# Kernel tuning notes

Hardware: AMD Instinct MI355X
Metric: run time of the kernel (lower is better)

## Reference

```python
import jax, jax.numpy as jnp
import numpy as np

KH = KW = 3
PAD = 1
SPE = 16  # msfa 4x4

def _unfold(x):
    # torch F.unfold order: feature index = c*(kh*kw) + di*kw + dj
    N, C, H, W = x.shape
    xp = jnp.pad(x, ((0, 0), (0, 0), (PAD, PAD), (PAD, PAD)))
    patches = jnp.stack(
        [xp[:, :, di:di + H, dj:dj + W] for di in range(KH) for dj in range(KW)],
        axis=2,
    )  # [N, C, KH*KW, H, W]
    return patches.reshape(N, C * KH * KW, H * W)

def setup_inputs() -> dict:
    key = jax.random.key(0)
    k1, k2 = jax.random.split(key)
    x = jax.random.normal(k1, (4, 32, 256, 256), dtype=jnp.float32)
    # kaiming_uniform(a=sqrt(5)) on fan_in = in_channels*kh*kw of the (spe,K,outC) tensor;
    # exact init distribution is irrelevant for correctness baseline, use scaled uniform.
    fan_in = 288
    bound = np.sqrt(6.0 / ((1 + 5) * fan_in))
    weight = jax.random.uniform(k2, (SPE, 288, 64), dtype=jnp.float32, minval=-bound, maxval=bound)
    return {"x": x, "weight": weight}

def reference(x, weight):
    N, C, H, W = x.shape
    spe, K, outC = weight.shape  # (16, 288, 64)
    cols = _unfold(x)                      # [N, K, HW]
    cols = jnp.transpose(cols, (0, 2, 1))  # [N, HW, K]
    G = (H * W) // spe
    colsg = cols.reshape(N, G, spe, K)     # position p uses weight[p % spe]
    out = jnp.einsum('ngsk,skc->ngsc', colsg, weight)  # [N, G, spe, outC]
    out = out.reshape(N, H, W, outC).transpose(0, 3, 1, 2)  # [N, outC, H, W]
    return out
```

## Files before the change

kernel.cpp:

```cpp
#include <hip/hip_runtime.h>
#include <hip/hip_bf16.h>


using bf16 = __hip_bfloat16;
typedef __attribute__((ext_vector_type(8))) short bf16x8_t;
typedef __attribute__((ext_vector_type(4))) float f32x4_t;

constexpr int NB    = 4;
constexpr int C_IN  = 32;
constexpr int HH    = 256;
constexpr int WW    = 256;
constexpr int C_OUT = 64;
constexpr int SPE   = 16;

constexpr int TH = 16;
constexpr int TW = 32;
constexpr int XR = TH + 2;
constexpr int XC = TW + 2;
constexpr int CPAD = 40;

__global__ __launch_bounds__(256)
void prep_weights(const float* __restrict__ w, bf16* __restrict__ wt) {
    int idx = blockIdx.x * 256 + threadIdx.x;
    if (idx >= SPE * C_OUT * 288) return;
    int s  = idx / (C_OUT * 288);
    int r  = idx % (C_OUT * 288);
    int co = r / 288;
    int kk = r % 288;
    int tap = kk >> 5;
    int c   = kk & 31;
    float v = w[((size_t)s * 288 + c * 9 + tap) * C_OUT + co];
    wt[idx] = __float2bfloat16(v);
}

__global__ __launch_bounds__(1024, 8)
void conv_mosaic_mfma(const float* __restrict__ x,
                      const bf16* __restrict__ wt,
                      float* __restrict__ out) {
    __shared__ __align__(16) bf16 xs[XR * XC * CPAD];

    const int n  = blockIdx.y;
    const int tw = blockIdx.x & 7;
    const int th = blockIdx.x >> 3;
    const int h0 = th * TH;
    const int w0 = tw * TW;
    const int t  = threadIdx.x;

    const float* xn = x + (size_t)n * C_IN * HH * WW;
    for (int idx = t; idx < C_IN * XR * XC; idx += 1024) {
        int c   = idx / (XR * XC);
        int rr  = idx % (XR * XC);
        int r   = rr / XC;
        int col = rr % XC;
        int gh = h0 + r - 1;
        int gw = w0 + col - 1;
        float v = 0.0f;
        if (gh >= 0 && gh < HH && gw >= 0 && gw < WW)
            v = xn[((size_t)c * HH + gh) * WW + gw];
        xs[(r * XC + col) * CPAD + c] = __float2bfloat16(v);
    }
    __syncthreads();

    const int wave = t >> 6;
    const int lane = t & 63;
    const int g    = wave & 3;
    const int ct   = wave >> 2;
    const int lm   = lane & 15;
    const int lg   = lane >> 4;

    f32x4_t dacc[2][4];
#pragma unroll
    for (int b = 0; b < 2; ++b)
#pragma unroll
        for (int c = 0; c < 4; ++c) dacc[b][c] = (f32x4_t){0.f, 0.f, 0.f, 0.f};

#pragma unroll
    for (int si = 0; si < 4; ++si) {
        const int s = g * 4 + si;
        const bf16* bp = wt + ((size_t)(s * C_OUT + ct * 16 + lm) * 288 + lg * 8);
        const bf16* ap = &xs[(lm * XC + s) * CPAD + lg * 8];
#pragma unroll
        for (int tap = 0; tap < 9; ++tap) {
            const int di = tap / 3, dj = tap % 3;
            bf16x8_t bfr = *reinterpret_cast<const bf16x8_t*>(bp + tap * 32);
            bf16x8_t a0 = *reinterpret_cast<const bf16x8_t*>(ap + (di * XC + dj) * CPAD);
            bf16x8_t a1 = *reinterpret_cast<const bf16x8_t*>(ap + (di * XC + dj + 16) * CPAD);
            dacc[0][si] = __builtin_amdgcn_mfma_f32_16x16x32_bf16(a0, bfr, dacc[0][si], 0, 0, 0);
            dacc[1][si] = __builtin_amdgcn_mfma_f32_16x16x32_bf16(a1, bfr, dacc[1][si], 0, 0, 0);
        }
    }

    const int co = ct * 16 + lm;
#pragma unroll
    for (int wm = 0; wm < 2; ++wm) {
#pragma unroll
        for (int j = 0; j < 4; ++j) {
            const int h = h0 + lg * 4 + j;
            float4 v = make_float4(dacc[wm][0][j], dacc[wm][1][j],
                                   dacc[wm][2][j], dacc[wm][3][j]);
            *reinterpret_cast<float4*>(
                &out[(((size_t)n * C_OUT + co) * HH + h) * WW + w0 + g * 4 + wm * 16]) = v;
        }
    }
}

extern "C" void kernel_launch(void* const* d_in, const int* in_sizes, int n_in,
                              void* d_out, int out_size, void* d_ws, size_t ws_size,
                              hipStream_t stream) {
    const float* x = (const float*)d_in[0];
    const float* w = (const float*)d_in[1];
    float* out     = (float*)d_out;
    bf16* wt       = (bf16*)d_ws;

    prep_weights<<<(SPE * C_OUT * 288 + 255) / 256, 256, 0, stream>>>(w, wt);

    dim3 grid((WW / TW) * (HH / TH), NB);
    conv_mosaic_mfma<<<grid, 1024, 0, stream>>>(x, wt, out);
}
```

Before: 64.47 us.

## Pre-convert input to padded NHWC bf16 and read it directly from global memory

```diff
diff --git a/kernel.cpp b/kernel.cpp
--- a/kernel.cpp
+++ b/kernel.cpp
@@ -13,11 +13,8 @@
 constexpr int C_OUT = 64;
 constexpr int SPE   = 16;
 
-constexpr int TH = 16;
-constexpr int TW = 32;
-constexpr int XR = TH + 2;
-constexpr int XC = TW + 2;
-constexpr int CPAD = 40;
+constexpr int HP = HH + 2;
+constexpr int WP = WW + 2;
 
 __global__ __launch_bounds__(256)
 void prep_weights(const float* __restrict__ w, bf16* __restrict__ wt) {
@@ -33,33 +30,45 @@
     wt[idx] = __float2bfloat16(v);
 }
 
-__global__ __launch_bounds__(1024, 8)
-void conv_mosaic_mfma(const float* __restrict__ x,
+__global__ __launch_bounds__(256)
+void prep_x(const float* __restrict__ x, bf16* __restrict__ xb) {
+    const int hp = blockIdx.x;
+    const int n  = blockIdx.y;
+    const int t  = threadIdx.x;
+    const int wl = t & 63;
+    const int c0 = (t >> 6) * 8;
+
+    const float* xn = x + (size_t)n * C_IN * HH * WW;
+    bf16* xr = xb + (((size_t)n * HP + hp) * WP) * C_IN;
+
+#pragma unroll
+    for (int it = 0; it < 5; ++it) {
+        const int wp = wl + it * 64;
+        if (wp < WP) {
+            const bool inb = (hp >= 1) && (hp <= HH) && (wp >= 1) && (wp <= WW);
+            union { bf16x8_t v; bf16 e[8]; } u;
+#pragma unroll
+            for (int j = 0; j < 8; ++j) {
+                float vv = 0.0f;
+                if (inb)
+                    vv = xn[((size_t)(c0 + j) * HH + (hp - 1)) * WW + (wp - 1)];
+                u.e[j] = __float2bfloat16(vv);
+            }
+            *reinterpret_cast<bf16x8_t*>(&xr[(size_t)wp * C_IN + c0]) = u.v;
+        }
+    }
+}
+
+__global__ __launch_bounds__(1024, 4)
+void conv_mosaic_mfma(const bf16* __restrict__ xb,
                       const bf16* __restrict__ wt,
                       float* __restrict__ out) {
-    __shared__ __align__(16) bf16 xs[XR * XC * CPAD];
-
     const int n  = blockIdx.y;
     const int tw = blockIdx.x & 7;
     const int th = blockIdx.x >> 3;
-    const int h0 = th * TH;
-    const int w0 = tw * TW;
+    const int h0 = th * 16;
+    const int w0 = tw * 32;
     const int t  = threadIdx.x;
-
-    const float* xn = x + (size_t)n * C_IN * HH * WW;
-    for (int idx = t; idx < C_IN * XR * XC; idx += 1024) {
-        int c   = idx / (XR * XC);
-        int rr  = idx % (XR * XC);
-        int r   = rr / XC;
-        int col = rr % XC;
-        int gh = h0 + r - 1;
-        int gw = w0 + col - 1;
-        float v = 0.0f;
-        if (gh >= 0 && gh < HH && gw >= 0 && gw < WW)
-            v = xn[((size_t)c * HH + gh) * WW + gw];
-        xs[(r * XC + col) * CPAD + c] = __float2bfloat16(v);
-    }
-    __syncthreads();
 
     const int wave = t >> 6;
     const int lane = t & 63;
@@ -67,6 +76,9 @@
     const int ct   = wave >> 2;
     const int lm   = lane & 15;
     const int lg   = lane >> 4;
+
+    const bf16* an = xb + (((size_t)n * HP + h0 + lm) * WP + (w0 + g * 4)) * C_IN + lg * 8;
+    const bf16* bpb = wt + ((size_t)(g * 4 * C_OUT + ct * 16 + lm) * 288 + lg * 8);
 
     f32x4_t dacc[2][4];
 #pragma unroll
@@ -76,17 +88,21 @@
 
 #pragma unroll
     for (int si = 0; si < 4; ++si) {
-        const int s = g * 4 + si;
-        const bf16* bp = wt + ((size_t)(s * C_OUT + ct * 16 + lm) * 288 + lg * 8);
-        const bf16* ap = &xs[(lm * XC + s) * CPAD + lg * 8];
+        bf16x8_t bfr[9];
+#pragma unroll
+        for (int tap = 0; tap < 9; ++tap)
+            bfr[tap] = *reinterpret_cast<const bf16x8_t*>(
+                bpb + (size_t)si * C_OUT * 288 + tap * 32);
+
 #pragma unroll
         for (int tap = 0; tap < 9; ++tap) {
             const int di = tap / 3, dj = tap % 3;
-            bf16x8_t bfr = *reinterpret_cast<const bf16x8_t*>(bp + tap * 32);
-            bf16x8_t a0 = *reinterpret_cast<const bf16x8_t*>(ap + (di * XC + dj) * CPAD);
-            bf16x8_t a1 = *reinterpret_cast<const bf16x8_t*>(ap + (di * XC + dj + 16) * CPAD);
-            dacc[0][si] = __builtin_amdgcn_mfma_f32_16x16x32_bf16(a0, bfr, dacc[0][si], 0, 0, 0);
-            dacc[1][si] = __builtin_amdgcn_mfma_f32_16x16x32_bf16(a1, bfr, dacc[1][si], 0, 0, 0);
+            bf16x8_t a0 = *reinterpret_cast<const bf16x8_t*>(
+                an + (di * WP + si + dj) * C_IN);
+            bf16x8_t a1 = *reinterpret_cast<const bf16x8_t*>(
+                an + (di * WP + si + dj + 16) * C_IN);
+            dacc[0][si] = __builtin_amdgcn_mfma_f32_16x16x32_bf16(a0, bfr[tap], dacc[0][si], 0, 0, 0);
+            dacc[1][si] = __builtin_amdgcn_mfma_f32_16x16x32_bf16(a1, bfr[tap], dacc[1][si], 0, 0, 0);
         }
     }
 
@@ -110,10 +126,13 @@
     const float* x = (const float*)d_in[0];
     const float* w = (const float*)d_in[1];
     float* out     = (float*)d_out;
-    bf16* wt       = (bf16*)d_ws;
+
+    bf16* wt = (bf16*)d_ws;
+    bf16* xb = (bf16*)((char*)d_ws + (1u << 20));
 
     prep_weights<<<(SPE * C_OUT * 288 + 255) / 256, 256, 0, stream>>>(w, wt);
+    prep_x<<<dim3(HP, NB), 256, 0, stream>>>(x, xb);
 
-    dim3 grid((WW / TW) * (HH / TH), NB);
-    conv_mosaic_mfma<<<grid, 1024, 0, stream>>>(x, wt, out);
+    dim3 grid((WW / 32) * (HH / 16), NB);
+    conv_mosaic_mfma<<<grid, 1024, 0, stream>>>(xb, wt, out);
 }
```

New measurement: 95.30 us. +47.8%, slower.
